# Kernel tuning notes

Measured on AMD Instinct MI355X. Metric: run time of the kernel, lower is better.

## Reference

```python
import jax, jax.numpy as jnp
import numpy as np

B, T, L, D, H = 64, 512, 2, 1024, 1024


def setup_inputs() -> dict:
    key = jax.random.key(0)
    ks = jax.random.split(key, 6)
    s = 1.0 / np.sqrt(H)
    return {
        "input_": jax.random.normal(ks[0], (B, T, D), dtype=jnp.float32),
        "hx": jnp.zeros((B, L, H), dtype=jnp.float32),
        "cx": jnp.zeros((B, L, H), dtype=jnp.float32),
        "W_ih": jax.random.uniform(ks[1], (L, 4 * H, D), minval=-s, maxval=s, dtype=jnp.float32),
        "W_hh": jax.random.uniform(ks[2], (L, 4 * H, H), minval=-s, maxval=s, dtype=jnp.float32),
        "b_ih": jax.random.uniform(ks[3], (L, 4 * H), minval=-s, maxval=s, dtype=jnp.float32),
        "b_hh": jax.random.uniform(ks[4], (L, 4 * H), minval=-s, maxval=s, dtype=jnp.float32),
    }


def _lstm_cell(x, h, c, wih, whh, bih, bhh):
    # gates: [B, 4H]
    gates = x @ wih.T + bih + h @ whh.T + bhh
    i, f, g, o = jnp.split(gates, 4, axis=-1)
    c_new = jax.nn.sigmoid(f) * c + jax.nn.sigmoid(i) * jnp.tanh(g)
    h_new = jax.nn.sigmoid(o) * jnp.tanh(c_new)
    return h_new, c_new


def reference(input_, hx, cx, W_ih, W_hh, b_ih, b_hh):
    num_layers = W_ih.shape[0]
    h0 = jnp.moveaxis(hx, 1, 0)  # [L, B, H]
    c0 = jnp.moveaxis(cx, 1, 0)  # [L, B, H]

    def step(carry, x_t):
        hs, cs = carry
        inp = x_t
        new_hs, new_cs = [], []
        for l in range(num_layers):  # fixed small layer count
            h, c = _lstm_cell(inp, hs[l], cs[l], W_ih[l], W_hh[l], b_ih[l], b_hh[l])
            new_hs.append(h)
            new_cs.append(c)
            inp = h  # dropout(p=0.0) is identity
        return (jnp.stack(new_hs), jnp.stack(new_cs)), inp

    (hT, cT), ys = jax.lax.scan(step, (h0, c0), jnp.moveaxis(input_, 1, 0))
    new_output = jnp.moveaxis(ys, 0, 1)  # [B, T, H]
    return new_output, (hT[-1], cT[-1])
```

## Files before the change

kernel.cpp:

```cpp
#include <hip/hip_runtime.h>

typedef __attribute__((ext_vector_type(8))) short s16x8;
typedef __attribute__((ext_vector_type(4))) float f32x4;
typedef __attribute__((ext_vector_type(2))) float f32x2;

#define B_ 64
#define T_ 512
#define H_ 1024
#define G4 4096
#define K2 2048
#define NPERS 256
#define WLDS_BYTES 131072
#define LDS_BYTES (WLDS_BYTES + 64 * 33 * 4)

__device__ __forceinline__ short f2bf(float f) {
  union { float f; unsigned u; } x; x.f = f;
  unsigned r = (x.u + 0x7fffu + ((x.u >> 16) & 1u)) >> 16;
  return (short)r;
}

__device__ __forceinline__ float fast_sigmoid(float x) {
  return 1.f / (1.f + __expf(-x));
}
__device__ __forceinline__ float fast_tanh(float x) {
  float e = __expf(-2.f * fabsf(x));
  float t = (1.f - e) / (1.f + e);
  return copysignf(t, x);
}

__device__ __forceinline__ s16x8 cohload(const short* p) {
  union { unsigned long long u[2]; s16x8 v; } x;
  unsigned long long* q = (unsigned long long*)p;
  x.u[0] = __hip_atomic_load(q,     __ATOMIC_RELAXED, __HIP_MEMORY_SCOPE_AGENT);
  x.u[1] = __hip_atomic_load(q + 1, __ATOMIC_RELAXED, __HIP_MEMORY_SCOPE_AGENT);
  return x.v;
}

__global__ void prep_kernel(const float* __restrict__ input_, const float* __restrict__ hx,
                            const float* __restrict__ cx, const float* __restrict__ W_ih,
                            const float* __restrict__ W_hh, const float* __restrict__ b_ih,
                            const float* __restrict__ b_hh,
                            short* __restrict__ Wp, float* __restrict__ bias,
                            short* __restrict__ Xp, short* __restrict__ h0buf,
                            short* __restrict__ h1buf, float* __restrict__ c0,
                            float* __restrict__ c1, unsigned* __restrict__ bar, int use_xbf)
{
  const long total = use_xbf ? 33554432L : 16777216L;
  for (long idx = (long)blockIdx.x * blockDim.x + threadIdx.x; idx < total;
       idx += (long)gridDim.x * blockDim.x) {
    if (use_xbf && idx < 33554432L) {
      int e = idx & 7;
      int b = (idx >> 3) & 63;
      long tc = idx >> 9;
      int c = (int)(tc & 127);
      int t = (int)(tc >> 7);
      Xp[idx] = f2bf(input_[((long)b * T_ + t) * H_ + c * 8 + e]);
    }
    if (idx < 16777216L) {
      int lb = (int)(idx >> 16);
      int layer = lb >> 7, nblk = lb & 127;
      int r = (int)(idx & 65535);
      int e = r & 7;
      int lane = (r >> 3) & 63;
      int fragiter = r >> 9;
      int frag = fragiter & 1, iter = fragiter >> 1;
      int n = frag * 16 + (lane & 15);
      int k = iter * 32 + (lane >> 4) * 8 + e;
      int j = (n >> 3) * H_ + nblk * 8 + (n & 7);
      float v = (k < H_) ? W_ih[((long)(layer << 12) + j) * H_ + k]
                         : W_hh[((long)(layer << 12) + j) * H_ + (k - H_)];
      Wp[idx] = f2bf(v);
    }
    if (idx < 8192) bias[idx] = b_ih[idx] + b_hh[idx];
    if (idx < 65536) {
      int b = (int)(idx >> 10), n = (int)(idx & 1023);
      int pi = (n >> 3) * 512 + b * 8 + (n & 7);
      h0buf[65536 + pi] = f2bf(hx[(b * 2 + 0) * H_ + n]);
      h1buf[65536 + pi] = f2bf(hx[(b * 2 + 1) * H_ + n]);
      c0[pi] = cx[(b * 2 + 0) * H_ + n];
      c1[pi] = cx[(b * 2 + 1) * H_ + n];
    }
    if (idx < 1024) bar[idx] = 0u;
  }
}


#define LOADQ(R, Q)                                                              \
  do {                                                                           \
    if ((Q) < 2) {                                                               \
      if (layer == 0) {                                                          \
        if (XBF) {                                                               \
          _Pragma("unroll") for (int j = 0; j < 16; j++)                         \
            R[j] = *(const s16x8*)(pAxl + ((Q) * 16 + j) * 2048);                \
        } else {                                                                 \
          _Pragma("unroll") for (int j = 0; j < 16; j++) {                       \
            const float* pp = xrow_f + ((Q) * 16 + j) * 32;                      \
            s16x8 tmp;                                                           \
            _Pragma("unroll") for (int e = 0; e < 8; e++) tmp[e] = f2bf(pp[e]);  \
            R[j] = tmp;                                                          \
          }                                                                      \
        }                                                                        \
      } else {                                                                   \
        _Pragma("unroll") for (int j = 0; j < 16; j++)                           \
          R[j] = cohload(pAxl + ((Q) * 16 + j) * 2048);                          \
      }                                                                          \
    } else {                                                                     \
      _Pragma("unroll") for (int j = 0; j < 16; j++)                             \
        R[j] = cohload(pAhl + (((Q) - 2) * 16 + j) * 2048);                      \
    }                                                                            \
  } while (0)

#define COMPQ(R, Q)                                                              \
  do {                                                                           \
    _Pragma("unroll") for (int j = 0; j < 16; j++) {                             \
      const int i_ = (Q) * 16 + j;                                               \
      s16x8 bf0 = *(const s16x8*)(wbase + i_ * 1024);                            \
      s16x8 bf1 = *(const s16x8*)(wbase + i_ * 1024 + 512);                      \
      acc0 = __builtin_amdgcn_mfma_f32_16x16x32_bf16(R[j], bf0, acc0, 0, 0, 0);  \
      acc1 = __builtin_amdgcn_mfma_f32_16x16x32_bf16(R[j], bf1, acc1, 0, 0, 0);  \
    }                                                                            \
  } while (0)

template <int XBF>
__global__ __launch_bounds__(256, 1)
void lstm_persist(const short* __restrict__ Wp, const float* __restrict__ b_ih,
                  const float* __restrict__ b_hh, const float* __restrict__ cx,
                  const short* __restrict__ Xp, const float* __restrict__ xf32,
                  short* __restrict__ h0buf, short* __restrict__ h1buf,
                  float* __restrict__ out, unsigned* bar)
{
  extern __shared__ char lds_raw[];
  short* wl = (short*)lds_raw;
  float (*gbuf)[33] = (float (*)[33])(lds_raw + WLDS_BYTES);

  const int blk = blockIdx.x;
  const int layer = blk >> 7;
  const int nblk = blk & 127;
  const int tid = threadIdx.x;
  const int lane = tid & 63;
  const int wave = tid >> 6;
  const int quad = lane >> 4;
  const int lo = lane & 15;
  const int n0 = nblk * 8;
  const int b = wave * 16 + lo;
  const int grp = blk >> 4;

  {
    const s16x8* src = (const s16x8*)(Wp + ((long)blk << 16));
    s16x8* dst = (s16x8*)wl;
    for (int i = tid; i < 8192; i += 256) dst[i] = src[i];
  }

  const int p0 = tid * 2;
  const int bb = p0 >> 3;
  const int nl = p0 & 7;
  const int n_a = n0 + nl, n_b = n_a + 1;
  float c_a = cx[(bb * 2 + layer) * H_ + n_a];
  float c_b = cx[(bb * 2 + layer) * H_ + n_b];
  const float* bia = b_ih + layer * G4;
  const float* bib = b_hh + layer * G4;
  const float bi_a = bia[n_a] + bib[n_a],             bi_b = bia[n_b] + bib[n_b];
  const float bf_a = bia[1024 + n_a] + bib[1024 + n_a], bf_b = bia[1024 + n_b] + bib[1024 + n_b];
  const float bg_a = bia[2048 + n_a] + bib[2048 + n_a], bg_b = bia[2048 + n_b] + bib[2048 + n_b];
  const float bo_a = bia[3072 + n_a] + bib[3072 + n_a], bo_b = bia[3072 + n_b] + bib[3072 + n_b];

  const short* wbase = wl + lane * 8;
  __syncthreads();

  for (int s = 0; s <= T_; s++) {
    const int active = (layer == 0) ? (s < T_) : (s > 0);
    if (active) {
      const int t = (layer == 0) ? s : (s - 1);
      const short* pAxl = nullptr;
      const float* xrow_f = nullptr;
      if (layer == 0) {
        if (XBF) pAxl = Xp + (long)t * 65536 + b * 8 + quad * 512;
        else     xrow_f = xf32 + ((long)b * T_ + t) * H_ + quad * 8;
      } else {
        pAxl = h0buf + ((s + 1) & 1) * 65536 + b * 8 + quad * 512;
      }
      const short* pAhl = (layer ? h1buf + (s & 1) * 65536
                                 : h0buf + ((s + 1) & 1) * 65536) + b * 8 + quad * 512;

      f32x4 acc0 = {0.f, 0.f, 0.f, 0.f}, acc1 = {0.f, 0.f, 0.f, 0.f};
      s16x8 ra[16], rb[16];

      LOADQ(ra, 0);
      LOADQ(rb, 1);
      COMPQ(ra, 0);
      LOADQ(ra, 2);
      COMPQ(rb, 1);
      LOADQ(rb, 3);
      COMPQ(ra, 2);
      COMPQ(rb, 3);

#pragma unroll
      for (int r = 0; r < 4; r++) {
        int m = wave * 16 + quad * 4 + r;
        gbuf[m][lo] = acc0[r];
        gbuf[m][16 + lo] = acc1[r];
      }
      __syncthreads();

      float ig_a = gbuf[bb][nl]          + bi_a, ig_b = gbuf[bb][nl + 1]      + bi_b;
      float fg_a = gbuf[bb][8 + nl]      + bf_a, fg_b = gbuf[bb][8 + nl + 1]  + bf_b;
      float gg_a = gbuf[bb][16 + nl]     + bg_a, gg_b = gbuf[bb][16 + nl + 1] + bg_b;
      float og_a = gbuf[bb][24 + nl]     + bo_a, og_b = gbuf[bb][24 + nl + 1] + bo_b;
      c_a = fast_sigmoid(fg_a) * c_a + fast_sigmoid(ig_a) * fast_tanh(gg_a);
      c_b = fast_sigmoid(fg_b) * c_b + fast_sigmoid(ig_b) * fast_tanh(gg_b);
      float hn_a = fast_sigmoid(og_a) * fast_tanh(c_a);
      float hn_b = fast_sigmoid(og_b) * fast_tanh(c_b);

      short* hdst = (layer ? h1buf : h0buf) + ((layer ? (s + 1) : s) & 1) * 65536 + nblk * 512;
      unsigned hp = (unsigned)(unsigned short)f2bf(hn_a)
                  | ((unsigned)(unsigned short)f2bf(hn_b) << 16);
      __hip_atomic_store((unsigned*)(hdst + p0), hp, __ATOMIC_RELAXED, __HIP_MEMORY_SCOPE_AGENT);

      if (layer) {
        long oi = ((long)bb * T_ + t) * H_ + n_a;
        f32x2 o2 = {hn_a, hn_b};
        __builtin_nontemporal_store(o2, (f32x2*)(out + oi));
        if (t == T_ - 1) {
          out[33554432L + bb * H_ + n_a] = hn_a;
          out[33554432L + bb * H_ + n_b] = hn_b;
          out[33554432L + 65536 + bb * H_ + n_a] = c_a;
          out[33554432L + 65536 + bb * H_ + n_b] = c_b;
        }
      }
    }

    if (s < T_) {
      __syncthreads();
      if (tid == 0) {
        unsigned old = __hip_atomic_fetch_add(&bar[grp * 32], 1u,
                                              __ATOMIC_RELAXED, __HIP_MEMORY_SCOPE_AGENT);
        if (old == (unsigned)(s * 16 + 15))
          __hip_atomic_fetch_add(&bar[512], 1u,
                                 __ATOMIC_RELAXED, __HIP_MEMORY_SCOPE_AGENT);
        const unsigned target = (unsigned)((s + 1) * 16);
        int tries = 0;
        while (__hip_atomic_load(&bar[512], __ATOMIC_RELAXED, __HIP_MEMORY_SCOPE_AGENT) < target) {
          __builtin_amdgcn_s_sleep(2);
          if (++tries > (1 << 20)) break;
        }
      }
      __syncthreads();
    }
  }
}

template <int XBF>
__global__ __launch_bounds__(256)
void lstm_step(const short* __restrict__ Wp, const float* __restrict__ bias,
               const short* __restrict__ Xp, const float* __restrict__ xf32,
               short* __restrict__ h0buf, short* __restrict__ h1buf,
               float* __restrict__ c0, float* __restrict__ c1,
               float* __restrict__ out, int s)
{
  const int blk = blockIdx.x;
  const int layer = blk >> 7;
  const int nblk = blk & 127;
  if (layer == 0 && s == T_) return;
  if (layer == 1 && s == 0) return;
  const int t = (layer == 0) ? s : (s - 1);

  const int lane = threadIdx.x & 63;
  const int wave = threadIdx.x >> 6;
  const int quad = lane >> 4;
  const int lo = lane & 15;
  const int n0 = nblk * 8;
  const int b = wave * 16 + lo;

  const short* baseX;
  const short* baseH;
  const float* xrow_f = nullptr;
  if (layer == 0) {
    baseX = Xp + (long)t * 65536;
    if (!XBF) xrow_f = xf32 + ((long)b * T_ + t) * H_;
    baseH = h0buf + ((s + 1) & 1) * 65536;
  } else {
    baseX = h0buf + ((s + 1) & 1) * 65536;
    baseH = h1buf + (s & 1) * 65536;
  }
  const short* pAx = baseX + b * 8;
  const short* pAh = baseH + b * 8;
  const short* wbase = Wp + ((long)(layer * 128 + nblk) << 16) + lane * 8;

  f32x4 acc0 = {0.f, 0.f, 0.f, 0.f}, acc1 = {0.f, 0.f, 0.f, 0.f};

#pragma unroll 4
  for (int k0 = 0; k0 < K2; k0 += 32) {
    const int koff = k0 + quad * 8;
    s16x8 af;
    if (koff < H_) {
      if (XBF || layer == 1) {
        af = *(const s16x8*)(pAx + koff * 64);
      } else {
        const float* p = xrow_f + koff;
        s16x8 tmp;
#pragma unroll
        for (int e = 0; e < 8; e++) tmp[e] = f2bf(p[e]);
        af = tmp;
      }
    } else {
      af = *(const s16x8*)(pAh + (koff - H_) * 64);
    }
    const s16x8 bf0 = *(const s16x8*)(wbase + k0 * 32);
    const s16x8 bf1 = *(const s16x8*)(wbase + k0 * 32 + 512);
    acc0 = __builtin_amdgcn_mfma_f32_16x16x32_bf16(af, bf0, acc0, 0, 0, 0);
    acc1 = __builtin_amdgcn_mfma_f32_16x16x32_bf16(af, bf1, acc1, 0, 0, 0);
  }

  __shared__ float gbuf[64][33];
#pragma unroll
  for (int r = 0; r < 4; r++) {
    int m = wave * 16 + quad * 4 + r;
    gbuf[m][lo] = acc0[r];
    gbuf[m][16 + lo] = acc1[r];
  }
  __syncthreads();

  float* cb = (layer ? c1 : c0) + nblk * 512;
  short* hdst = (layer ? h1buf : h0buf) + ((layer ? (s + 1) : s) & 1) * 65536 + nblk * 512;
  const float* bl = bias + layer * G4;

  for (int p = threadIdx.x; p < 512; p += 256) {
    int bb = p >> 3, nl = p & 7;
    int nn = n0 + nl;
    float ig = gbuf[bb][nl]      + bl[nn];
    float fg = gbuf[bb][8 + nl]  + bl[1024 + nn];
    float gg = gbuf[bb][16 + nl] + bl[2048 + nn];
    float og = gbuf[bb][24 + nl] + bl[3072 + nn];
    float cp = cb[p];
    float si = fast_sigmoid(ig);
    float sf = fast_sigmoid(fg);
    float so = fast_sigmoid(og);
    float cn = sf * cp + si * fast_tanh(gg);
    float hn = so * fast_tanh(cn);
    cb[p] = cn;
    hdst[p] = f2bf(hn);
    if (layer) {
      out[((long)bb * T_ + t) * H_ + nn] = hn;
      if (t == T_ - 1) {
        out[33554432L + bb * H_ + nn] = hn;
        out[33554432L + 65536 + bb * H_ + nn] = cn;
      }
    }
  }
}

extern "C" void kernel_launch(void* const* d_in, const int* in_sizes, int n_in,
                              void* d_out, int out_size, void* d_ws, size_t ws_size,
                              hipStream_t stream)
{
  const float* input_ = (const float*)d_in[0];
  const float* hx   = (const float*)d_in[1];
  const float* cx   = (const float*)d_in[2];
  const float* W_ih = (const float*)d_in[3];
  const float* W_hh = (const float*)d_in[4];
  const float* b_ih = (const float*)d_in[5];
  const float* b_hh = (const float*)d_in[6];
  float* out = (float*)d_out;

  char* w = (char*)d_ws;
  size_t off = 0;
  short* Wp  = (short*)(w + off); off += 33554432;
  float* bias = (float*)(w + off); off += 32768;
  size_t state_bytes = 4 * 262144 + 4096;
  int use_xbf = (ws_size >= off + 67108864 + state_bytes) ? 1 : 0;
  short* Xp = nullptr;
  if (use_xbf) { Xp = (short*)(w + off); off += 67108864; }
  short* h0buf = (short*)(w + off); off += 262144;
  short* h1buf = (short*)(w + off); off += 262144;
  float* c0 = (float*)(w + off); off += 262144;
  float* c1 = (float*)(w + off); off += 262144;
  unsigned* bar = (unsigned*)(w + off); off += 4096;

  hipLaunchKernelGGL(prep_kernel, dim3(4096), dim3(256), 0, stream,
                     input_, hx, cx, W_ih, W_hh, b_ih, b_hh,
                     Wp, bias, Xp, h0buf, h1buf, c0, c1, bar, use_xbf);

  auto f1 = &lstm_persist<1>;
  auto f0 = &lstm_persist<0>;
  static int attr_done = 0;
  if (!attr_done) {
    (void)hipFuncSetAttribute(reinterpret_cast<const void*>(f1),
                              hipFuncAttributeMaxDynamicSharedMemorySize, LDS_BYTES);
    (void)hipFuncSetAttribute(reinterpret_cast<const void*>(f0),
                              hipFuncAttributeMaxDynamicSharedMemorySize, LDS_BYTES);
    attr_done = 1;
  }

  void* args[] = {(void*)&Wp, (void*)&b_ih, (void*)&b_hh, (void*)&cx,
                  (void*)&Xp, (void*)&input_, (void*)&h0buf, (void*)&h1buf,
                  (void*)&out, (void*)&bar};
  hipError_t ce;
  if (use_xbf) {
    ce = hipLaunchCooperativeKernel(f1, dim3(NPERS), dim3(256), args,
                                    (unsigned)LDS_BYTES, stream);
  } else {
    ce = hipLaunchCooperativeKernel(f0, dim3(NPERS), dim3(256), args,
                                    (unsigned)LDS_BYTES, stream);
  }
  if (ce != hipSuccess) {
    if (use_xbf) {
      for (int s = 0; s <= T_; s++)
        hipLaunchKernelGGL((lstm_step<1>), dim3(256), dim3(256), 0, stream,
                           Wp, bias, Xp, input_, h0buf, h1buf, c0, c1, out, s);
    } else {
      for (int s = 0; s <= T_; s++)
        hipLaunchKernelGGL((lstm_step<0>), dim3(256), dim3(256), 0, stream,
                           Wp, bias, Xp, input_, h0buf, h1buf, c0, c1, out, s);
    }
  }
}
```

Before: 5.146 ms.

## Store full per-step hidden-state history to read with plain loads

Adds per-layer history buffers holding the bf16 hidden state for every timestep, used when the workspace is large enough. Each step writes to a fresh slice instead of a double buffer, so later reads can use ordinary vector loads rather than agent-scope atomic coherent loads. Since no address is ever rewritten, stale cached lines cannot hold old data. This costs about 134 MB of extra workspace, and it relies on non-coherent loads seeing the other blocks' atomic stores after the barrier.

After: 11.07 ms. 115% more time.

```diff
diff --git a/kernel.cpp b/kernel.cpp
--- a/kernel.cpp
+++ b/kernel.cpp
@@ -12,6 +12,7 @@
 #define NPERS 256
 #define WLDS_BYTES 131072
 #define LDS_BYTES (WLDS_BYTES + 64 * 33 * 4)
+#define HIST_SLICES 514
 
 __device__ __forceinline__ short f2bf(float f) {
   union { float f; unsigned u; } x; x.f = f;
@@ -43,7 +44,9 @@
                             short* __restrict__ Wp, float* __restrict__ bias,
                             short* __restrict__ Xp, short* __restrict__ h0buf,
                             short* __restrict__ h1buf, float* __restrict__ c0,
-                            float* __restrict__ c1, unsigned* __restrict__ bar, int use_xbf)
+                            float* __restrict__ c1, unsigned* __restrict__ bar,
+                            short* __restrict__ hist0, short* __restrict__ hist1,
+                            int use_xbf, int use_hist)
 {
   const long total = use_xbf ? 33554432L : 16777216L;
   for (long idx = (long)blockIdx.x * blockDim.x + threadIdx.x; idx < total;
@@ -75,8 +78,14 @@
     if (idx < 65536) {
       int b = (int)(idx >> 10), n = (int)(idx & 1023);
       int pi = (n >> 3) * 512 + b * 8 + (n & 7);
-      h0buf[65536 + pi] = f2bf(hx[(b * 2 + 0) * H_ + n]);
-      h1buf[65536 + pi] = f2bf(hx[(b * 2 + 1) * H_ + n]);
+      short i0 = f2bf(hx[(b * 2 + 0) * H_ + n]);
+      short i1 = f2bf(hx[(b * 2 + 1) * H_ + n]);
+      h0buf[65536 + pi] = i0;
+      h1buf[65536 + pi] = i1;
+      if (use_hist) {
+        hist0[pi] = i0;
+        hist1[65536 + pi] = i1;
+      }
       c0[pi] = cx[(b * 2 + 0) * H_ + n];
       c1[pi] = cx[(b * 2 + 1) * H_ + n];
     }
@@ -85,29 +94,31 @@
 }
 
 
-#define LOADQ(R, Q)                                                              \
+#define UNR16 _Pragma("unroll") for (int j = 0; j < 16; j++)
+
+#define LQX(R, Q)                                                                \
   do {                                                                           \
-    if ((Q) < 2) {                                                               \
-      if (layer == 0) {                                                          \
-        if (XBF) {                                                               \
-          _Pragma("unroll") for (int j = 0; j < 16; j++)                         \
-            R[j] = *(const s16x8*)(pAxl + ((Q) * 16 + j) * 2048);                \
-        } else {                                                                 \
-          _Pragma("unroll") for (int j = 0; j < 16; j++) {                       \
-            const float* pp = xrow_f + ((Q) * 16 + j) * 32;                      \
-            s16x8 tmp;                                                           \
-            _Pragma("unroll") for (int e = 0; e < 8; e++) tmp[e] = f2bf(pp[e]);  \
-            R[j] = tmp;                                                          \
-          }                                                                      \
+    if (layer == 0) {                                                            \
+      if (XBF) {                                                                 \
+        UNR16 R[j] = *(const s16x8*)(pAxl + ((Q) * 16 + j) * 2048);              \
+      } else {                                                                   \
+        UNR16 {                                                                  \
+          const float* pp = xrow_f + ((Q) * 16 + j) * 32;                        \
+          s16x8 tmp;                                                             \
+          _Pragma("unroll") for (int e = 0; e < 8; e++) tmp[e] = f2bf(pp[e]);    \
+          R[j] = tmp;                                                            \
         }                                                                        \
-      } else {                                                                   \
-        _Pragma("unroll") for (int j = 0; j < 16; j++)                           \
-          R[j] = cohload(pAxl + ((Q) * 16 + j) * 2048);                          \
       }                                                                          \
     } else {                                                                     \
-      _Pragma("unroll") for (int j = 0; j < 16; j++)                             \
-        R[j] = cohload(pAhl + (((Q) - 2) * 16 + j) * 2048);                      \
+      if (HIST) { UNR16 R[j] = *(const s16x8*)(pAxl + ((Q) * 16 + j) * 2048); }  \
+      else      { UNR16 R[j] = cohload(pAxl + ((Q) * 16 + j) * 2048); }          \
     }                                                                            \
+  } while (0)
+
+#define LQH(R, Q2)                                                               \
+  do {                                                                           \
+    if (HIST) { UNR16 R[j] = *(const s16x8*)(pAhl + ((Q2) * 16 + j) * 2048); }   \
+    else      { UNR16 R[j] = cohload(pAhl + ((Q2) * 16 + j) * 2048); }           \
   } while (0)
 
 #define COMPQ(R, Q)                                                              \
@@ -121,12 +132,13 @@
     }                                                                            \
   } while (0)
 
-template <int XBF>
+template <int XBF, int HIST>
 __global__ __launch_bounds__(256, 1)
 void lstm_persist(const short* __restrict__ Wp, const float* __restrict__ b_ih,
                   const float* __restrict__ b_hh, const float* __restrict__ cx,
                   const short* __restrict__ Xp, const float* __restrict__ xf32,
                   short* __restrict__ h0buf, short* __restrict__ h1buf,
+                  short* __restrict__ hist0, short* __restrict__ hist1,
                   float* __restrict__ out, unsigned* bar)
 {
   extern __shared__ char lds_raw[];
@@ -171,26 +183,28 @@
     const int active = (layer == 0) ? (s < T_) : (s > 0);
     if (active) {
       const int t = (layer == 0) ? s : (s - 1);
+      const long sl = (long)s * 65536;
       const short* pAxl = nullptr;
+      const short* pAhl;
       const float* xrow_f = nullptr;
       if (layer == 0) {
         if (XBF) pAxl = Xp + (long)t * 65536 + b * 8 + quad * 512;
         else     xrow_f = xf32 + ((long)b * T_ + t) * H_ + quad * 8;
+        pAhl = (HIST ? hist0 + sl : h0buf + ((s + 1) & 1) * 65536) + b * 8 + quad * 512;
       } else {
-        pAxl = h0buf + ((s + 1) & 1) * 65536 + b * 8 + quad * 512;
-      }
-      const short* pAhl = (layer ? h1buf + (s & 1) * 65536
-                                 : h0buf + ((s + 1) & 1) * 65536) + b * 8 + quad * 512;
+        pAxl = (HIST ? hist0 + sl : h0buf + ((s + 1) & 1) * 65536) + b * 8 + quad * 512;
+        pAhl = (HIST ? hist1 + sl : h1buf + (s & 1) * 65536) + b * 8 + quad * 512;
+      }
 
       f32x4 acc0 = {0.f, 0.f, 0.f, 0.f}, acc1 = {0.f, 0.f, 0.f, 0.f};
       s16x8 ra[16], rb[16];
 
-      LOADQ(ra, 0);
-      LOADQ(rb, 1);
+      LQX(ra, 0);
+      LQX(rb, 1);
       COMPQ(ra, 0);
-      LOADQ(ra, 2);
+      LQH(ra, 0);
       COMPQ(rb, 1);
-      LOADQ(rb, 3);
+      LQH(rb, 1);
       COMPQ(ra, 2);
       COMPQ(rb, 3);
 
@@ -211,7 +225,9 @@
       float hn_a = fast_sigmoid(og_a) * fast_tanh(c_a);
       float hn_b = fast_sigmoid(og_b) * fast_tanh(c_b);
 
-      short* hdst = (layer ? h1buf : h0buf) + ((layer ? (s + 1) : s) & 1) * 65536 + nblk * 512;
+      short* hdst;
+      if (HIST) hdst = (layer ? hist1 : hist0) + (long)(s + 1) * 65536 + nblk * 512;
+      else      hdst = (layer ? h1buf : h0buf) + ((layer ? (s + 1) : s) & 1) * 65536 + nblk * 512;
       unsigned hp = (unsigned)(unsigned short)f2bf(hn_a)
                   | ((unsigned)(unsigned short)f2bf(hn_b) << 16);
       __hip_atomic_store((unsigned*)(hdst + p0), hp, __ATOMIC_RELAXED, __HIP_MEMORY_SCOPE_AGENT);
@@ -362,44 +378,65 @@
   const float* b_hh = (const float*)d_in[6];
   float* out = (float*)d_out;
 
+  const size_t WPB = 33554432, BIASB = 32768, XPB = 67108864;
+  const size_t HB = 262144, CB = 262144, BARB = 4096;
+  const size_t HISTB = (size_t)HIST_SLICES * 65536 * 2;
+
+  const size_t tier2 = WPB + BIASB + XPB + 2 * HB + 2 * CB + BARB;
+  const size_t tier3 = tier2 + 2 * HISTB;
+
+  int use_xbf  = (ws_size >= tier2) ? 1 : 0;
+  int use_hist = (ws_size >= tier3) ? 1 : 0;
+
   char* w = (char*)d_ws;
   size_t off = 0;
-  short* Wp  = (short*)(w + off); off += 33554432;
-  float* bias = (float*)(w + off); off += 32768;
-  size_t state_bytes = 4 * 262144 + 4096;
-  int use_xbf = (ws_size >= off + 67108864 + state_bytes) ? 1 : 0;
+  short* Wp  = (short*)(w + off); off += WPB;
+  float* bias = (float*)(w + off); off += BIASB;
   short* Xp = nullptr;
-  if (use_xbf) { Xp = (short*)(w + off); off += 67108864; }
-  short* h0buf = (short*)(w + off); off += 262144;
-  short* h1buf = (short*)(w + off); off += 262144;
-  float* c0 = (float*)(w + off); off += 262144;
-  float* c1 = (float*)(w + off); off += 262144;
-  unsigned* bar = (unsigned*)(w + off); off += 4096;
+  if (use_xbf) { Xp = (short*)(w + off); off += XPB; }
+  short* h0buf = (short*)(w + off); off += HB;
+  short* h1buf = (short*)(w + off); off += HB;
+  float* c0 = (float*)(w + off); off += CB;
+  float* c1 = (float*)(w + off); off += CB;
+  unsigned* bar = (unsigned*)(w + off); off += BARB;
+  short* hist0 = nullptr;
+  short* hist1 = nullptr;
+  if (use_hist) {
+    hist0 = (short*)(w + off); off += HISTB;
+    hist1 = (short*)(w + off); off += HISTB;
+  }
 
   hipLaunchKernelGGL(prep_kernel, dim3(4096), dim3(256), 0, stream,
                      input_, hx, cx, W_ih, W_hh, b_ih, b_hh,
-                     Wp, bias, Xp, h0buf, h1buf, c0, c1, bar, use_xbf);
-
-  auto f1 = &lstm_persist<1>;
-  auto f0 = &lstm_persist<0>;
+                     Wp, bias, Xp, h0buf, h1buf, c0, c1, bar, hist0, hist1,
+                     use_xbf, use_hist);
+
+  auto f11 = &lstm_persist<1, 1>;
+  auto f10 = &lstm_persist<1, 0>;
+  auto f00 = &lstm_persist<0, 0>;
   static int attr_done = 0;
   if (!attr_done) {
-    (void)hipFuncSetAttribute(reinterpret_cast<const void*>(f1),
+    (void)hipFuncSetAttribute(reinterpret_cast<const void*>(f11),
                               hipFuncAttributeMaxDynamicSharedMemorySize, LDS_BYTES);
-    (void)hipFuncSetAttribute(reinterpret_cast<const void*>(f0),
+    (void)hipFuncSetAttribute(reinterpret_cast<const void*>(f10),
+                              hipFuncAttributeMaxDynamicSharedMemorySize, LDS_BYTES);
+    (void)hipFuncSetAttribute(reinterpret_cast<const void*>(f00),
                               hipFuncAttributeMaxDynamicSharedMemorySize, LDS_BYTES);
     attr_done = 1;
   }
 
   void* args[] = {(void*)&Wp, (void*)&b_ih, (void*)&b_hh, (void*)&cx,
                   (void*)&Xp, (void*)&input_, (void*)&h0buf, (void*)&h1buf,
-                  (void*)&out, (void*)&bar};
+                  (void*)&hist0, (void*)&hist1, (void*)&out, (void*)&bar};
   hipError_t ce;
-  if (use_xbf) {
-    ce = hipLaunchCooperativeKernel(f1, dim3(NPERS), dim3(256), args,
+  if (use_hist) {
+    ce = hipLaunchCooperativeKernel(f11, dim3(NPERS), dim3(256), args,
+                                    (unsigned)LDS_BYTES, stream);
+  } else if (use_xbf) {
+    ce = hipLaunchCooperativeKernel(f10, dim3(NPERS), dim3(256), args,
                                     (unsigned)LDS_BYTES, stream);
   } else {
-    ce = hipLaunchCooperativeKernel(f0, dim3(NPERS), dim3(256), args,
+    ce = hipLaunchCooperativeKernel(f00, dim3(NPERS), dim3(256), args,
                                     (unsigned)LDS_BYTES, stream);
   }
   if (ce != hipSuccess) {
```
